# Optimization experiments

Measured on AMD Instinct MI355X. Metric: run time of the kernel, lower is better.

Reference implementation:

```python
import jax, jax.numpy as jnp
import numpy as np

# ---- config (mirrors __init__ / spec) ----
ANCHORS = jnp.array([[0.57273, 0.677385], [1.87446, 2.06253], [3.33843, 5.47434],
                     [7.88282, 3.52778], [9.77052, 9.16828]], dtype=jnp.float32)
A = 5            # num_anchors
C = 80           # num_classes
MAX_OBJ = 50
NOOBJ_SCALE = 1.0
OBJ_SCALE = 5.0
IGNORE_THR = 0.6
COORD_SCALE = 1.0
CLASS_SCALE = 1.0


def _iou(cx1, cy1, w1, h1, cx2, cy2, w2, h2):
    """IoU for center-format boxes (is_corner_coordinates=False), broadcasting."""
    mx = jnp.minimum(cx1 - w1 * 0.5, cx2 - w2 * 0.5)
    Mx = jnp.maximum(cx1 + w1 * 0.5, cx2 + w2 * 0.5)
    my = jnp.minimum(cy1 - h1 * 0.5, cy2 - h2 * 0.5)
    My = jnp.maximum(cy1 + h1 * 0.5, cy2 + h2 * 0.5)
    cw = w1 + w2 - (Mx - mx)
    ch = h1 + h2 - (My - my)
    inter = jnp.where((cw > 0) & (ch > 0), cw * ch, 0.0)
    union = w1 * h1 + w2 * h2 - inter
    return jnp.where(union > 0, inter / union, 0.0)


def _build_targets(pred_boxes, tgt, Hf, Wf):
    """Vectorized version of YOLOv2Loss._build_targets.
    pred_boxes: (B,A,H,W,4) detached boxes in feature-map units.
    tgt: (B,T,5) = [class, cx, cy, w, h] normalized; cx==-1 terminates.
    """
    B, T = tgt.shape[0], tgt.shape[1]
    cls_gt, cx, cy, wn, hn = (tgt[..., k] for k in range(5))
    # loop breaks at first cx==-1 -> cumulative validity
    valid = jnp.cumprod((cx != -1.0).astype(jnp.int32), axis=1).astype(bool)  # (B,T)
    gx, gy, gw, gh = cx * Wf, cy * Hf, wn * Wf, hn * Hf

    # --- pass 1: noobj mask from max IoU of every pred box vs every gt box ---
    pb = pred_boxes[:, None]  # (B,1,A,H,W,4)
    ious = _iou(pb[..., 0], pb[..., 1], pb[..., 2], pb[..., 3],
                gx[:, :, None, None, None], gy[:, :, None, None, None],
                gw[:, :, None, None, None], gh[:, :, None, None, None])  # (B,T,A,H,W)
    ious = jnp.where(valid[:, :, None, None, None], ious, 0.0)
    max_iou = ious.max(axis=1)                                   # (B,A,H,W)
    noobj_pre = (max_iou <= IGNORE_THR).astype(jnp.float32)

    # --- pass 2: best anchor per gt via shape-only IoU (0,0,w,h) ---
    a_iou = _iou(0.0, 0.0, gw[..., None], gh[..., None],
                 0.0, 0.0, ANCHORS[:, 0], ANCHORS[:, 1])          # (B,T,A)
    best_n = jnp.argmax(a_iou, axis=-1)                           # (B,T)
    gi = jnp.clip(gx.astype(jnp.int32), 0, Wf - 1)
    gj = jnp.clip(gy.astype(jnp.int32), 0, Hf - 1)

    N = B * A * Hf * Wf
    b_idx = jnp.arange(B)[:, None]
    flat = ((b_idx * A + best_n) * Hf + gj) * Wf + gi             # (B,T)
    flat = jnp.where(valid, flat, N)                              # OOB sentinel -> dropped
    flat1 = flat.reshape(-1)

    # tconf = IoU(gt box, predicted box at assigned cell)
    pb_flat = pred_boxes.reshape(N, 4)
    sel = pb_flat[jnp.clip(flat1, 0, N - 1)].reshape(B, T, 4)
    tconf_v = _iou(gx, gy, gw, gh, sel[..., 0], sel[..., 1], sel[..., 2], sel[..., 3])

    aw = ANCHORS[best_n, 0]
    ah = ANCHORS[best_n, 1]
    tw_v = jnp.log(jnp.where(valid, gw / aw, 1.0))
    th_v = jnp.log(jnp.where(valid, gh / ah, 1.0))
    tx_v = gx - gi
    ty_v = gy - gj

    def scat(vals):
        return jnp.zeros(N, jnp.float32).at[flat1].set(
            vals.reshape(-1), mode='drop').reshape(B, A, Hf, Wf)

    obj = scat(jnp.ones((B, T), jnp.float32))
    noobj = noobj_pre * (1.0 - obj)
    return (obj, noobj, scat(tx_v), scat(ty_v), scat(tw_v), scat(th_v),
            scat(tconf_v), scat(cls_gt))


def yolo_loss(predictions, target):
    B, _, Hf, Wf = predictions.shape
    out = predictions.reshape(B, A, 5 + C, Hf, Wf)
    x = jax.nn.sigmoid(out[:, :, 0])
    y = jax.nn.sigmoid(out[:, :, 1])
    w = out[:, :, 2]
    h = out[:, :, 3]
    conf = jax.nn.sigmoid(out[:, :, 4])
    cls_logits = out[:, :, 5:]                                    # (B,A,C,H,W)

    grid_x = jnp.arange(Wf, dtype=jnp.float32)
    grid_y = jnp.arange(Hf, dtype=jnp.float32)[:, None]
    bx = x + grid_x
    by = y + grid_y
    bw = jnp.exp(w) * ANCHORS[:, 0][None, :, None, None]
    bh = jnp.exp(h) * ANCHORS[:, 1][None, :, None, None]
    # original operates on .data -> detached
    pred_boxes = jax.lax.stop_gradient(jnp.stack([bx, by, bw, bh], axis=-1))

    tgt = target.reshape(B, MAX_OBJ, 5)
    obj, noobj, tx, ty, tw, th, tconf, tcls = _build_targets(pred_boxes, tgt, Hf, Wf)

    # coord + confidence losses: reduction='sum'
    loss_coord = COORD_SCALE * jnp.sum(
        obj * ((x - tx) ** 2 + (y - ty) ** 2 + (w - tw) ** 2 + (h - th) ** 2))
    conf_mask = OBJ_SCALE * obj + NOOBJ_SCALE * noobj
    loss_conf = jnp.sum(conf_mask * (conf - tconf) ** 2)

    # class loss: cross-entropy over obj cells, reduction='mean'
    logp = jax.nn.log_softmax(cls_logits, axis=2)                 # (B,A,C,H,W)
    ce = -jnp.take_along_axis(logp, tcls.astype(jnp.int32)[:, :, None], axis=2)[:, :, 0]
    n_obj = jnp.maximum(jnp.sum(obj), 1.0)
    loss_cls = CLASS_SCALE * jnp.sum(obj * ce) / n_obj
    return loss_coord + loss_conf + loss_cls


def setup_inputs() -> dict:
    key = jax.random.key(0)
    k1, k2, k3, k4, k5 = jax.random.split(key, 5)
    B, Hf, Wf = 64, 38, 38
    predictions = jax.random.normal(k1, (B, A * (5 + C), Hf, Wf), jnp.float32) * 0.5
    n_obj = jax.random.randint(k2, (B,), 1, 21)
    cls = jax.random.randint(k3, (B, MAX_OBJ), 0, C).astype(jnp.float32)
    cxy = jax.random.uniform(k4, (B, MAX_OBJ, 2), minval=0.05, maxval=0.95)
    wh = jax.random.uniform(k5, (B, MAX_OBJ, 2), minval=0.05, maxval=0.4)
    tgt = jnp.concatenate([cls[..., None], cxy, wh], axis=-1)      # (B,T,5)
    valid = jnp.arange(MAX_OBJ)[None, :] < n_obj[:, None]
    pad = jnp.array([0.0, -1.0, 0.0, 0.0, 0.0], jnp.float32)       # cx=-1 terminates
    tgt = jnp.where(valid[..., None], tgt, pad)
    return {"predictions": predictions, "target": tgt.reshape(B, MAX_OBJ * 5)}


def reference(predictions, target):
    return yolo_loss(predictions, target)
```

## Files before the change

### kernel.cpp

```cpp
#include <hip/hip_runtime.h>
#include <math.h>

#define NB 64
#define NA 5
#define NC 80
#define HH 38
#define WW 38
#define HW (HH*WW)
#define CELLS (NA*HW)
#define NT 50
#define NCH 85
#define MBLK 29

#define WS_PART 0
#define WS_CLSP (NB*MBLK)
#define WS_NOBJ (NB*MBLK + NB)

__constant__ float c_aw[NA] = {0.57273f, 1.87446f, 3.33843f, 7.88282f, 9.77052f};
__constant__ float c_ah[NA] = {0.677385f, 2.06253f, 5.47434f, 3.52778f, 9.16828f};

__global__ __launch_bounds__(256) void yolo_fused(const float* __restrict__ pred,
                                                  const float* __restrict__ tgt,
                                                  float* __restrict__ ws) {
    const int b   = blockIdx.y;
    const int bx  = blockIdx.x;
    const int tid = threadIdx.x;

    __shared__ float s_gx[NT], s_gy[NT], s_gw[NT], s_gh[NT];
    __shared__ float s_tx[NT], s_ty[NT], s_tw[NT], s_th[NT];
    __shared__ int   s_cell[NT], s_cls[NT];
    __shared__ int   s_vc;
    __shared__ float s_red[4];

    if (tid < 64) {
        float cls = 0.f, cx = -1.f, cy = 0.f, wn = 0.f, hn = 0.f;
        if (tid < NT) {
            const float* tr = tgt + ((size_t)b*NT + tid)*5;
            cls = tr[0]; cx = tr[1]; cy = tr[2]; wn = tr[3]; hn = tr[4];
        }
        unsigned long long inv = __ballot(cx == -1.0f);
        const int vc = (int)__ffsll(inv) - 1;
        if (tid == 0) s_vc = vc;
        if (tid < vc) {
            float gx = cx*WW, gy = cy*HH, gw = wn*WW, gh = hn*HH;
            int best = 0; float bi = -1.0f;
            #pragma unroll
            for (int a = 0; a < NA; ++a) {
                float inter = fminf(gw, c_aw[a]) * fminf(gh, c_ah[a]);
                float un = gw*gh + c_aw[a]*c_ah[a] - inter;
                float iou = (un > 0.f) ? inter/un : 0.f;
                if (iou > bi) { bi = iou; best = a; }
            }
            int gi = (int)gx; gi = gi < 0 ? 0 : (gi > WW-1 ? WW-1 : gi);
            int gj = (int)gy; gj = gj < 0 ? 0 : (gj > HH-1 ? HH-1 : gj);
            s_gx[tid] = gx; s_gy[tid] = gy; s_gw[tid] = gw; s_gh[tid] = gh;
            s_tx[tid] = gx - (float)gi; s_ty[tid] = gy - (float)gj;
            s_tw[tid] = logf(gw / c_aw[best]);
            s_th[tid] = logf(gh / c_ah[best]);
            s_cell[tid] = (best*HH + gj)*WW + gi;
            s_cls[tid]  = (int)cls;
        }
    }
    __syncthreads();
    const int vc = s_vc;

    if (bx < MBLK) {
        float l = 0.f;
        const int cell = bx * 256 + tid;
        if (cell < CELLS) {
            const int a   = cell / HW;
            const int rem = cell - a*HW;
            const int j   = rem / WW;
            const int i   = rem - j*WW;
            const float* base = pred + ((size_t)(b*(NA*NCH) + a*NCH))*HW + rem;
            float p0 = base[0];
            float p1 = base[HW];
            float p2 = base[2*HW];
            float p3 = base[3*HW];
            float p4 = base[4*HW];
            float x    = 1.f/(1.f + expf(-p0));
            float y    = 1.f/(1.f + expf(-p1));
            float conf = 1.f/(1.f + expf(-p4));
            float bxx = x + (float)i;
            float byy = y + (float)j;
            float bw = expf(p2) * c_aw[a];
            float bh = expf(p3) * c_ah[a];
            float hbw = bw*0.5f, hbh = bh*0.5f;
            float pa = bw*bh;

            float maxiou = 0.f, miou = 0.f;
            int match = -1;
            for (int t = 0; t < vc; ++t) {
                float gx = s_gx[t], gy = s_gy[t], gw = s_gw[t], gh = s_gh[t];
                float mx = fminf(bxx - hbw, gx - gw*0.5f);
                float Mx = fmaxf(bxx + hbw, gx + gw*0.5f);
                float my = fminf(byy - hbh, gy - gh*0.5f);
                float My = fmaxf(byy + hbh, gy + gh*0.5f);
                float cw  = bw + gw - (Mx - mx);
                float chh = bh + gh - (My - my);
                float inter = (cw > 0.f && chh > 0.f) ? cw*chh : 0.f;
                float un = pa + gw*gh - inter;
                float iou = (un > 0.f) ? inter/un : 0.f;
                maxiou = fmaxf(maxiou, iou);
                if (s_cell[t] == cell) { match = t; miou = iou; }
            }

            if (match >= 0) {
                float dx = x  - s_tx[match];
                float dy = y  - s_ty[match];
                float dw = p2 - s_tw[match];
                float dh = p3 - s_th[match];
                l += dx*dx + dy*dy + dw*dw + dh*dh;
                float dc = conf - miou;
                l += 5.0f * dc*dc;
            } else if (maxiou <= 0.6f) {
                l += conf*conf;
            }
        }

        #pragma unroll
        for (int off = 32; off > 0; off >>= 1) l += __shfl_down(l, off, 64);
        if ((tid & 63) == 0) s_red[tid >> 6] = l;
        __syncthreads();
        if (tid == 0)
            ws[WS_PART + b*MBLK + bx] = s_red[0]+s_red[1]+s_red[2]+s_red[3];
    } else {
        const int lane = tid & 63;
        const int wv   = tid >> 6;

        __shared__ int s_act[NT];
        __shared__ float s_nobj;
        if (tid < 64) {
            int active = 0;
            if (tid < vc) {
                active = 1;
                const int mycell = s_cell[tid];
                for (int u = tid+1; u < vc; ++u)
                    if (s_cell[u] == mycell) { active = 0; break; }
                s_act[tid] = active;
            }
            unsigned long long am = __ballot(active != 0);
            if (tid == 0) s_nobj = (float)__popcll(am);
        }
        __syncthreads();

        float csum = 0.f;
        for (int t = wv; t < vc; t += 4) {
            if (!s_act[t]) continue;
            const int cell = s_cell[t];
            const int a = cell / HW, rem = cell - a*HW;
            const float* logit = pred + ((size_t)(b*(NA*NCH) + a*NCH) + 5)*HW + rem;
            float v0 = logit[(size_t)lane*HW];
            float v1 = (lane < NC-64) ? logit[(size_t)(lane+64)*HW] : -INFINITY;
            float m = fmaxf(v0, v1);
            #pragma unroll
            for (int off = 32; off > 0; off >>= 1) m = fmaxf(m, __shfl_xor(m, off, 64));
            const int tc = s_cls[t];
            float s  = expf(v0 - m) + ((lane < NC-64) ? expf(v1 - m) : 0.f);
            float tl = ((lane == tc) ? v0 : 0.f) + ((lane + 64 == tc) ? v1 : 0.f);
            #pragma unroll
            for (int off = 32; off > 0; off >>= 1) {
                s  += __shfl_xor(s,  off, 64);
                tl += __shfl_xor(tl, off, 64);
            }
            csum += (m + logf(s)) - tl;
        }
        if (lane == 0) s_red[wv] = csum;
        __syncthreads();
        if (tid == 0) {
            ws[WS_CLSP + b] = s_red[0]+s_red[1]+s_red[2]+s_red[3];
            ws[WS_NOBJ + b] = s_nobj;
        }
    }
}

__global__ __launch_bounds__(256) void fin_k(const float* __restrict__ ws,
                                             float* __restrict__ out) {
    const int tid = threadIdx.x;
    __shared__ float s_red[4*3];
    float m = 0.f, c = 0.f, n = 0.f;
    for (int idx = tid; idx < NB*MBLK; idx += 256) m += ws[WS_PART + idx];
    if (tid < NB) { c = ws[WS_CLSP + tid]; n = ws[WS_NOBJ + tid]; }
    #pragma unroll
    for (int off = 32; off > 0; off >>= 1) {
        m += __shfl_down(m, off, 64);
        c += __shfl_down(c, off, 64);
        n += __shfl_down(n, off, 64);
    }
    const int wv = tid >> 6;
    if ((tid & 63) == 0) { s_red[wv*3] = m; s_red[wv*3+1] = c; s_red[wv*3+2] = n; }
    __syncthreads();
    if (tid == 0) {
        float M = 0.f, Cs = 0.f, Ns = 0.f;
        #pragma unroll
        for (int w = 0; w < 4; ++w) { M += s_red[w*3]; Cs += s_red[w*3+1]; Ns += s_red[w*3+2]; }
        out[0] = M + Cs / fmaxf(Ns, 1.0f);
    }
}

extern "C" void kernel_launch(void* const* d_in, const int* in_sizes, int n_in,
                              void* d_out, int out_size, void* d_ws, size_t ws_size,
                              hipStream_t stream) {
    const float* pred = (const float*)d_in[0];
    const float* tgt  = (const float*)d_in[1];
    float* ws  = (float*)d_ws;
    float* out = (float*)d_out;

    hipLaunchKernelGGL(yolo_fused, dim3(MBLK+1, NB), dim3(256), 0, stream, pred, tgt, ws);
    hipLaunchKernelGGL(fin_k, dim3(1), dim3(256), 0, stream, ws, out);
}
```

Before: 199.4 us.

## Fuse final reduction into main kernel via atomics and last-block finalize

Drops the separate finalize kernel. Each block now atomically adds its partial sums into workspace accumulators, and the last block to finish, found through an atomic counter, writes the output. The workspace is zeroed with a memset before launch. Exact expf calls are also replaced by the fast __expf intrinsic. This trades one kernel launch for a memset plus atomic contention, and the float atomic accumulation order becomes nondeterministic.

```diff
diff --git a/kernel.cpp b/kernel.cpp
--- a/kernel.cpp
+++ b/kernel.cpp
@@ -11,17 +11,16 @@
 #define NT 50
 #define NCH 85
 #define MBLK 29
+#define TOTBLK ((MBLK+1)*NB)
 
-#define WS_PART 0
-#define WS_CLSP (NB*MBLK)
-#define WS_NOBJ (NB*MBLK + NB)
 
 __constant__ float c_aw[NA] = {0.57273f, 1.87446f, 3.33843f, 7.88282f, 9.77052f};
 __constant__ float c_ah[NA] = {0.677385f, 2.06253f, 5.47434f, 3.52778f, 9.16828f};
 
-__global__ __launch_bounds__(256) void yolo_fused(const float* __restrict__ pred,
-                                                  const float* __restrict__ tgt,
-                                                  float* __restrict__ ws) {
+__global__ __launch_bounds__(256) void yolo_one(const float* __restrict__ pred,
+                                                const float* __restrict__ tgt,
+                                                float* __restrict__ ws,
+                                                float* __restrict__ out) {
     const int b   = blockIdx.y;
     const int bx  = blockIdx.x;
     const int tid = threadIdx.x;
@@ -78,13 +77,13 @@
             float p2 = base[2*HW];
             float p3 = base[3*HW];
             float p4 = base[4*HW];
-            float x    = 1.f/(1.f + expf(-p0));
-            float y    = 1.f/(1.f + expf(-p1));
-            float conf = 1.f/(1.f + expf(-p4));
+            float x    = 1.f/(1.f + __expf(-p0));
+            float y    = 1.f/(1.f + __expf(-p1));
+            float conf = 1.f/(1.f + __expf(-p4));
             float bxx = x + (float)i;
             float byy = y + (float)j;
-            float bw = expf(p2) * c_aw[a];
-            float bh = expf(p3) * c_ah[a];
+            float bw = __expf(p2) * c_aw[a];
+            float bh = __expf(p3) * c_ah[a];
             float hbw = bw*0.5f, hbh = bh*0.5f;
             float pa = bw*bh;
 
@@ -123,7 +122,7 @@
         if ((tid & 63) == 0) s_red[tid >> 6] = l;
         __syncthreads();
         if (tid == 0)
-            ws[WS_PART + b*MBLK + bx] = s_red[0]+s_red[1]+s_red[2]+s_red[3];
+            atomicAdd(&ws[0], s_red[0]+s_red[1]+s_red[2]+s_red[3]);
     } else {
         const int lane = tid & 63;
         const int wv   = tid >> 6;
@@ -156,7 +155,7 @@
             #pragma unroll
             for (int off = 32; off > 0; off >>= 1) m = fmaxf(m, __shfl_xor(m, off, 64));
             const int tc = s_cls[t];
-            float s  = expf(v0 - m) + ((lane < NC-64) ? expf(v1 - m) : 0.f);
+            float s  = __expf(v0 - m) + ((lane < NC-64) ? __expf(v1 - m) : 0.f);
             float tl = ((lane == tc) ? v0 : 0.f) + ((lane + 64 == tc) ? v1 : 0.f);
             #pragma unroll
             for (int off = 32; off > 0; off >>= 1) {
@@ -168,33 +167,22 @@
         if (lane == 0) s_red[wv] = csum;
         __syncthreads();
         if (tid == 0) {
-            ws[WS_CLSP + b] = s_red[0]+s_red[1]+s_red[2]+s_red[3];
-            ws[WS_NOBJ + b] = s_nobj;
+            atomicAdd(&ws[1], s_red[0]+s_red[1]+s_red[2]+s_red[3]);
+            atomicAdd(&ws[2], s_nobj);
         }
     }
-}
 
-__global__ __launch_bounds__(256) void fin_k(const float* __restrict__ ws,
-                                             float* __restrict__ out) {
-    const int tid = threadIdx.x;
-    __shared__ float s_red[4*3];
-    float m = 0.f, c = 0.f, n = 0.f;
-    for (int idx = tid; idx < NB*MBLK; idx += 256) m += ws[WS_PART + idx];
-    if (tid < NB) { c = ws[WS_CLSP + tid]; n = ws[WS_NOBJ + tid]; }
-    #pragma unroll
-    for (int off = 32; off > 0; off >>= 1) {
-        m += __shfl_down(m, off, 64);
-        c += __shfl_down(c, off, 64);
-        n += __shfl_down(n, off, 64);
-    }
-    const int wv = tid >> 6;
-    if ((tid & 63) == 0) { s_red[wv*3] = m; s_red[wv*3+1] = c; s_red[wv*3+2] = n; }
-    __syncthreads();
     if (tid == 0) {
-        float M = 0.f, Cs = 0.f, Ns = 0.f;
-        #pragma unroll
-        for (int w = 0; w < 4; ++w) { M += s_red[w*3]; Cs += s_red[w*3+1]; Ns += s_red[w*3+2]; }
-        out[0] = M + Cs / fmaxf(Ns, 1.0f);
+        __threadfence();
+        unsigned* cnt = (unsigned*)&ws[3];
+        unsigned done = atomicAdd(cnt, 1u);
+        if (done == (unsigned)(TOTBLK - 1)) {
+            __threadfence();
+            float M  = atomicAdd(&ws[0], 0.0f);
+            float Cs = atomicAdd(&ws[1], 0.0f);
+            float Ns = atomicAdd(&ws[2], 0.0f);
+            out[0] = M + Cs / fmaxf(Ns, 1.0f);
+        }
     }
 }
 
@@ -206,6 +194,6 @@
     float* ws  = (float*)d_ws;
     float* out = (float*)d_out;
 
-    hipLaunchKernelGGL(yolo_fused, dim3(MBLK+1, NB), dim3(256), 0, stream, pred, tgt, ws);
-    hipLaunchKernelGGL(fin_k, dim3(1), dim3(256), 0, stream, ws, out);
+    hipMemsetAsync(d_ws, 0, 16, stream);
+    hipLaunchKernelGGL(yolo_one, dim3(MBLK+1, NB), dim3(256), 0, stream, pred, tgt, ws, out);
 }
```

Result: slower. 259.6 us (+30.2%).
